# Performance work log

Measured on AMD Instinct MI355X. Metric: run time of the kernel, lower is better.

Reference implementation:

```python
import jax, jax.numpy as jnp
import numpy as np

NUM_HEADS = 8


def setup_inputs() -> dict:
    key = jax.random.key(0)
    k1, k2, k3, k4 = jax.random.split(key, 4)
    C = 256
    x = jax.random.normal(k1, (1, C, 16, 16, 16), dtype=jnp.float32)
    qkv_w = jax.random.normal(k2, (3 * C, C), dtype=jnp.float32) * (C ** -0.5)
    proj_w = jax.random.normal(k3, (C, C), dtype=jnp.float32) * (C ** -0.5)
    proj_b = jax.random.normal(k4, (C,), dtype=jnp.float32) * 0.02
    return {"x": x, "qkv_w": qkv_w, "proj_w": proj_w, "proj_b": proj_b}


def reference(x, qkv_w, proj_w, proj_b):
    B, C, H, W, D = x.shape
    N = H * W * D
    nh = NUM_HEADS
    hd = C // nh
    scale = hd ** -0.5

    xf = x.reshape(B, C, N)
    # 1x1x1 Conv3d == pointwise linear over channel dim
    qkv = jnp.einsum('oc,bcn->bon', qkv_w, xf)           # [B, 3C, N]
    qkv = qkv.reshape(B, 3, nh, hd, N)
    q, k, v = qkv[:, 0], qkv[:, 1], qkv[:, 2]            # each [B, nh, hd, N]

    # q @ k^T over head_dim: scores [B, nh, N, N]
    attn = jnp.einsum('bhdn,bhdm->bhnm', q, k) * scale
    attn = jax.nn.softmax(attn, axis=-1)

    # (attn @ v) then transpose(2,3): result laid out as [B, nh, hd, N]
    out = jnp.einsum('bhnm,bhdm->bhdn', attn, v)
    out = out.reshape(B, C, N)

    out = jnp.einsum('oc,bcn->bon', proj_w, out) + proj_b[None, :, None]
    return out.reshape(B, C, H, W, D)
```

## Files before the change

### kernel.cpp

```cpp
#include <hip/hip_runtime.h>
#include <hip/hip_bf16.h>

typedef short short8 __attribute__((ext_vector_type(8)));
typedef unsigned short ushort8 __attribute__((ext_vector_type(8)));
typedef float f32x4 __attribute__((ext_vector_type(4)));
typedef unsigned int u32x4 __attribute__((ext_vector_type(4)));

#define MFMA16(a, b, c) __builtin_amdgcn_mfma_f32_16x16x32_bf16(a, b, c, 0, 0, 0)

__device__ __forceinline__ unsigned short f2bf(float f) {
    unsigned int u = __float_as_uint(f);
    unsigned int r = (u + 0x7fffu + ((u >> 16) & 1u)) >> 16;
    return (unsigned short)r;
}

__device__ __forceinline__ float fexp2(float x) {
#if __has_builtin(__builtin_amdgcn_exp2f)
    return __builtin_amdgcn_exp2f(x);
#else
    return exp2f(x);
#endif
}

__device__ __forceinline__ unsigned int cvtpk(float lo, float hi) {
    unsigned int r;
    asm("v_cvt_pk_bf16_f32 %0, %1, %2" : "=v"(r) : "v"(lo), "v"(hi));
    return r;
}

__device__ __forceinline__ float hsum4(f32x4 a) { return (a[0] + a[1]) + (a[2] + a[3]); }

#define QSC (0.17677669529663687f * 1.4426950408889634f)

__global__ __launch_bounds__(256) void k_prep(const float* __restrict__ qkv_w,
                                              const float* __restrict__ proj_w,
                                              const float* __restrict__ x,
                                              unsigned short* __restrict__ wqb,
                                              unsigned short* __restrict__ pwb,
                                              unsigned short* __restrict__ xtb) {
    __shared__ float lds[64][65];
    int t = threadIdx.x;
    if (blockIdx.x < 256) {
        int i = (blockIdx.x * 256 + t) * 4;
        const int NQ = 768 * 256;
        const float* src;
        unsigned short* dst;
        if (i < NQ) { src = qkv_w + i; dst = wqb + i; }
        else        { src = proj_w + (i - NQ); dst = pwb + (i - NQ); }
        float4 v = *reinterpret_cast<const float4*>(src);
        ushort4 p;
        p.x = f2bf(v.x); p.y = f2bf(v.y); p.z = f2bf(v.z); p.w = f2bf(v.w);
        *reinterpret_cast<ushort4*>(dst) = p;
        return;
    }
    int bid = blockIdx.x - 256;
    int nt = bid & 63;
    int ct = bid >> 6;
    {
        int cc = t >> 2, nseg = t & 3;
        const float* src = x + (ct * 64 + cc) * 4096 + nt * 64 + nseg * 16;
#pragma unroll
        for (int k2 = 0; k2 < 4; ++k2) {
            float4 v = *reinterpret_cast<const float4*>(src + 4 * k2);
            lds[cc][nseg * 16 + 4 * k2 + 0] = v.x;
            lds[cc][nseg * 16 + 4 * k2 + 1] = v.y;
            lds[cc][nseg * 16 + 4 * k2 + 2] = v.z;
            lds[cc][nseg * 16 + 4 * k2 + 3] = v.w;
        }
    }
    __syncthreads();
    {
        int nn = t >> 2, seg = t & 3;
        unsigned short o[16];
#pragma unroll
        for (int j = 0; j < 16; ++j) o[j] = f2bf(lds[seg * 16 + j][nn]);
        unsigned short* dst = xtb + (nt * 64 + nn) * 256 + ct * 64 + seg * 16;
#pragma unroll
        for (int k2 = 0; k2 < 4; ++k2) {
            ushort4 p;
            p.x = o[4 * k2 + 0]; p.y = o[4 * k2 + 1]; p.z = o[4 * k2 + 2]; p.w = o[4 * k2 + 3];
            *reinterpret_cast<ushort4*>(dst + 4 * k2) = p;
        }
    }
}

__global__ __launch_bounds__(256) void k_qkv(const unsigned short* __restrict__ wqb,
                                             const unsigned short* __restrict__ xtb,
                                             unsigned short* __restrict__ qws,
                                             unsigned short* __restrict__ kws,
                                             unsigned short* __restrict__ vws) {
    int nt = blockIdx.x;
    int ot = blockIdx.y;
    int w = threadIdx.x >> 6;
    int l = threadIdx.x & 63;
    int lr = l & 15, lg = l >> 4;
    int obase = ot * 128 + w * 32;
    int nbase = nt * 64;

    f32x4 acc[2][4];
#pragma unroll
    for (int mi = 0; mi < 2; ++mi)
#pragma unroll
        for (int ni = 0; ni < 4; ++ni) acc[mi][ni] = (f32x4){0.f, 0.f, 0.f, 0.f};

#pragma unroll
    for (int ks = 0; ks < 8; ++ks) {
        short8 a[2], b[4];
#pragma unroll
        for (int mi = 0; mi < 2; ++mi)
            a[mi] = *reinterpret_cast<const short8*>(wqb + (obase + mi * 16 + lr) * 256 + ks * 32 + lg * 8);
#pragma unroll
        for (int ni = 0; ni < 4; ++ni)
            b[ni] = *reinterpret_cast<const short8*>(xtb + (nbase + ni * 16 + lr) * 256 + ks * 32 + lg * 8);
#pragma unroll
        for (int mi = 0; mi < 2; ++mi)
#pragma unroll
            for (int ni = 0; ni < 4; ++ni)
                acc[mi][ni] = MFMA16(a[mi], b[ni], acc[mi][ni]);
    }

#pragma unroll
    for (int mi = 0; mi < 2; ++mi) {
        int o0 = obase + mi * 16 + lg * 4;
#pragma unroll
        for (int ni = 0; ni < 4; ++ni) {
            int n = nbase + ni * 16 + lr;
            f32x4 v = acc[mi][ni];
            if (o0 < 512) {
                float sc = (o0 < 256) ? QSC : 1.0f;
                unsigned short* base = (o0 < 256) ? qws : kws;
                int oo = o0 & 255;
                int h = oo >> 5, d0 = oo & 31;
                ushort4 pk;
                pk.x = f2bf(v[0] * sc); pk.y = f2bf(v[1] * sc);
                pk.z = f2bf(v[2] * sc); pk.w = f2bf(v[3] * sc);
                *reinterpret_cast<ushort4*>(base + h * 131072 + n * 32 + d0) = pk;
            } else {
                int oo = o0 - 512;
#pragma unroll
                for (int r = 0; r < 4; ++r) vws[(oo + r) * 4096 + n] = f2bf(v[r]);
            }
        }
    }
}

__global__ __launch_bounds__(256, 4) void k_attn(const unsigned short* __restrict__ qws,
                                                 const unsigned short* __restrict__ kws,
                                                 const unsigned short* __restrict__ vws,
                                                 float* __restrict__ opart,
                                                 float* __restrict__ oml) {
    __shared__ __align__(16) unsigned short sbuf[4096];

    int h  = blockIdx.x;
    int qs = blockIdx.y;
    int sp = blockIdx.z;
    int t = threadIdx.x;
    int w = t >> 6, l = t & 63, lr = l & 15, lg = l >> 4;

    const unsigned short* qh = qws + h * 131072;
    const unsigned short* kh = kws + h * 131072;
    const unsigned short* vh = vws + h * 131072;

    int qb = qs * 128 + w * 32;
    short8 bq0 = *reinterpret_cast<const short8*>(qh + (qb + lr) * 32 + lg * 8);
    short8 bq1 = *reinterpret_cast<const short8*>(qh + (qb + 16 + lr) * 32 + lg * 8);

    f32x4 o00 = {0.f,0.f,0.f,0.f}, o01 = o00, o10 = o00, o11 = o00;
    f32x4 la0 = {0.f,0.f,0.f,0.f}, la1 = {0.f,0.f,0.f,0.f};

    int krow_s = 8 * (lr >> 2) + (lr & 3) + 4 * (w & 1) + 32 * (w >> 1);
    const unsigned short* ksrc = kh + krow_s * 32 + lg * 8;
    unsigned short* kslot = &sbuf[w * 512 + l * 8];
    const unsigned short* vsrc = vh + ((w & 1) * 16 + lr) * 4096 + (w >> 1) * 32 + lg * 8;
    unsigned short* vslot = &sbuf[2048 + w * 512 + l * 8];

    int mt0 = sp * 16, mt1 = mt0 + 16;

    ushort8 kreg = *reinterpret_cast<const ushort8*>(ksrc + mt0 * 2048);
    ushort8 vreg = *reinterpret_cast<const ushort8*>(vsrc + mt0 * 64);

    for (int mt = mt0; mt < mt1; ++mt) {
        __syncthreads();
        *reinterpret_cast<ushort8*>(kslot) = kreg;
        *reinterpret_cast<ushort8*>(vslot) = vreg;
        __syncthreads();

        if (mt + 1 < mt1) {
            kreg = *reinterpret_cast<const ushort8*>(ksrc + (mt + 1) * 2048);
            vreg = *reinterpret_cast<const ushort8*>(vsrc + (mt + 1) * 64);
        }

        const unsigned short* kb = sbuf;
        short8 ka0 = *reinterpret_cast<const short8*>(kb + l * 8);
        short8 ka1 = *reinterpret_cast<const short8*>(kb + 512 + l * 8);
        short8 ka2 = *reinterpret_cast<const short8*>(kb + 1024 + l * 8);
        short8 ka3 = *reinterpret_cast<const short8*>(kb + 1536 + l * 8);
        const unsigned short* vbp = kb + 2048;
        short8 va00 = *reinterpret_cast<const short8*>(vbp + l * 8);
        short8 va10 = *reinterpret_cast<const short8*>(vbp + 512 + l * 8);
        short8 va01 = *reinterpret_cast<const short8*>(vbp + 1024 + l * 8);
        short8 va11 = *reinterpret_cast<const short8*>(vbp + 1536 + l * 8);

        const f32x4 z = {0.f, 0.f, 0.f, 0.f};
        f32x4 s00 = MFMA16(ka0, bq0, z);
        f32x4 s01 = MFMA16(ka1, bq0, z);
        f32x4 s02 = MFMA16(ka2, bq0, z);
        f32x4 s03 = MFMA16(ka3, bq0, z);
        f32x4 s10 = MFMA16(ka0, bq1, z);
        f32x4 s11 = MFMA16(ka1, bq1, z);
        f32x4 s12 = MFMA16(ka2, bq1, z);
        f32x4 s13 = MFMA16(ka3, bq1, z);

#pragma unroll
        for (int e = 0; e < 4; ++e) {
            s00[e] = fexp2(s00[e]); s01[e] = fexp2(s01[e]);
            s02[e] = fexp2(s02[e]); s03[e] = fexp2(s03[e]);
        }
        la0 += (s00 + s01) + (s02 + s03);
        union { u32x4 u; short8 s8; } p00, p01, p10, p11;
        p00.u[0] = cvtpk(s00[0], s00[1]); p00.u[1] = cvtpk(s00[2], s00[3]);
        p00.u[2] = cvtpk(s01[0], s01[1]); p00.u[3] = cvtpk(s01[2], s01[3]);
        p01.u[0] = cvtpk(s02[0], s02[1]); p01.u[1] = cvtpk(s02[2], s02[3]);
        p01.u[2] = cvtpk(s03[0], s03[1]); p01.u[3] = cvtpk(s03[2], s03[3]);

#pragma unroll
        for (int e = 0; e < 4; ++e) {
            s10[e] = fexp2(s10[e]); s11[e] = fexp2(s11[e]);
            s12[e] = fexp2(s12[e]); s13[e] = fexp2(s13[e]);
        }
        la1 += (s10 + s11) + (s12 + s13);
        p10.u[0] = cvtpk(s10[0], s10[1]); p10.u[1] = cvtpk(s10[2], s10[3]);
        p10.u[2] = cvtpk(s11[0], s11[1]); p10.u[3] = cvtpk(s11[2], s11[3]);
        p11.u[0] = cvtpk(s12[0], s12[1]); p11.u[1] = cvtpk(s12[2], s12[3]);
        p11.u[2] = cvtpk(s13[0], s13[1]); p11.u[3] = cvtpk(s13[2], s13[3]);

        o00 = MFMA16(va00, p00.s8, o00);
        o00 = MFMA16(va01, p01.s8, o00);
        o01 = MFMA16(va10, p00.s8, o01);
        o01 = MFMA16(va11, p01.s8, o01);
        o10 = MFMA16(va00, p10.s8, o10);
        o10 = MFMA16(va01, p11.s8, o10);
        o11 = MFMA16(va10, p10.s8, o11);
        o11 = MFMA16(va11, p11.s8, o11);
    }

    float ls0 = hsum4(la0);
    ls0 += __shfl_xor(ls0, 16);
    ls0 += __shfl_xor(ls0, 32);
    float ls1 = hsum4(la1);
    ls1 += __shfl_xor(ls1, 16);
    ls1 += __shfl_xor(ls1, 32);

    int q0 = qb + lr, q1 = qb + 16 + lr;
    float* ob0 = opart + ((h * 4096 + q0) * 4 + sp) * 32;
    float* ob1 = opart + ((h * 4096 + q1) * 4 + sp) * 32;
    __builtin_nontemporal_store(o00, reinterpret_cast<f32x4*>(ob0 + lg * 4));
    __builtin_nontemporal_store(o01, reinterpret_cast<f32x4*>(ob0 + 16 + lg * 4));
    __builtin_nontemporal_store(o10, reinterpret_cast<f32x4*>(ob1 + lg * 4));
    __builtin_nontemporal_store(o11, reinterpret_cast<f32x4*>(ob1 + 16 + lg * 4));
    oml[(h * 4096 + q0) * 4 + sp] = ls0;
    oml[(h * 4096 + q1) * 4 + sp] = ls1;
}

__global__ __launch_bounds__(256) void k_comb(const float* __restrict__ opart,
                                              const float* __restrict__ oml,
                                              unsigned short* __restrict__ ao) {
    int t = blockIdx.x * 256 + threadIdx.x;
    int hq = t >> 2;
    int dg = (t & 3) * 8;
    f32x4 lv = *reinterpret_cast<const f32x4*>(oml + hq * 4);
    float inv = 1.0f / ((lv[0] + lv[1]) + (lv[2] + lv[3]));

    const float* ob = opart + hq * 128 + dg;
    f32x4 v0 = __builtin_nontemporal_load(reinterpret_cast<const f32x4*>(ob));
    f32x4 v1 = __builtin_nontemporal_load(reinterpret_cast<const f32x4*>(ob + 32));
    f32x4 v2 = __builtin_nontemporal_load(reinterpret_cast<const f32x4*>(ob + 64));
    f32x4 v3 = __builtin_nontemporal_load(reinterpret_cast<const f32x4*>(ob + 96));
    f32x4 acc0 = (v0 + v1) + (v2 + v3);
    v0 = __builtin_nontemporal_load(reinterpret_cast<const f32x4*>(ob + 4));
    v1 = __builtin_nontemporal_load(reinterpret_cast<const f32x4*>(ob + 36));
    v2 = __builtin_nontemporal_load(reinterpret_cast<const f32x4*>(ob + 68));
    v3 = __builtin_nontemporal_load(reinterpret_cast<const f32x4*>(ob + 100));
    f32x4 acc1 = (v0 + v1) + (v2 + v3);

    int h = hq >> 12, q = hq & 4095;
    unsigned short* dst = ao + q * 256 + h * 32 + dg;
    ushort4 pk;
    pk.x = f2bf(acc0[0] * inv); pk.y = f2bf(acc0[1] * inv);
    pk.z = f2bf(acc0[2] * inv); pk.w = f2bf(acc0[3] * inv);
    *reinterpret_cast<ushort4*>(dst) = pk;
    pk.x = f2bf(acc1[0] * inv); pk.y = f2bf(acc1[1] * inv);
    pk.z = f2bf(acc1[2] * inv); pk.w = f2bf(acc1[3] * inv);
    *reinterpret_cast<ushort4*>(dst + 4) = pk;
}

__global__ __launch_bounds__(256) void k_proj(const unsigned short* __restrict__ pwb,
                                              const unsigned short* __restrict__ ao,
                                              const float* __restrict__ bias,
                                              float* __restrict__ out) {
    int nt = blockIdx.x;
    int ot = blockIdx.y;
    int w = threadIdx.x >> 6;
    int l = threadIdx.x & 63;
    int lr = l & 15, lg = l >> 4;
    int obase = ot * 128 + w * 32;
    int nbase = nt * 64;

    f32x4 acc[2][4];
#pragma unroll
    for (int mi = 0; mi < 2; ++mi)
#pragma unroll
        for (int ni = 0; ni < 4; ++ni) acc[mi][ni] = (f32x4){0.f, 0.f, 0.f, 0.f};

#pragma unroll
    for (int ks = 0; ks < 8; ++ks) {
        short8 a[2], b[4];
#pragma unroll
        for (int mi = 0; mi < 2; ++mi)
            a[mi] = *reinterpret_cast<const short8*>(pwb + (obase + mi * 16 + lr) * 256 + ks * 32 + lg * 8);
#pragma unroll
        for (int ni = 0; ni < 4; ++ni)
            b[ni] = *reinterpret_cast<const short8*>(ao + (nbase + ni * 16 + lr) * 256 + ks * 32 + lg * 8);
#pragma unroll
        for (int mi = 0; mi < 2; ++mi)
#pragma unroll
            for (int ni = 0; ni < 4; ++ni)
                acc[mi][ni] = MFMA16(a[mi], b[ni], acc[mi][ni]);
    }

#pragma unroll
    for (int mi = 0; mi < 2; ++mi) {
        int o0 = obase + mi * 16 + lg * 4;
        float b0 = bias[o0 + 0], b1 = bias[o0 + 1], b2 = bias[o0 + 2], b3 = bias[o0 + 3];
#pragma unroll
        for (int ni = 0; ni < 4; ++ni) {
            int n = nbase + ni * 16 + lr;
            out[(o0 + 0) * 4096 + n] = acc[mi][ni][0] + b0;
            out[(o0 + 1) * 4096 + n] = acc[mi][ni][1] + b1;
            out[(o0 + 2) * 4096 + n] = acc[mi][ni][2] + b2;
            out[(o0 + 3) * 4096 + n] = acc[mi][ni][3] + b3;
        }
    }
}

extern "C" void kernel_launch(void* const* d_in, const int* in_sizes, int n_in,
                              void* d_out, int out_size, void* d_ws, size_t ws_size,
                              hipStream_t stream) {
    const float* x      = (const float*)d_in[0];
    const float* qkv_w  = (const float*)d_in[1];
    const float* proj_w = (const float*)d_in[2];
    const float* proj_b = (const float*)d_in[3];
    float* out = (float*)d_out;

    char* ws = (char*)d_ws;
    unsigned short* wqb = (unsigned short*)(ws + 0);
    unsigned short* pwb = (unsigned short*)(ws + 393216);
    unsigned short* xtb = (unsigned short*)(ws + 524288);
    unsigned short* qws = (unsigned short*)(ws + 2621440);
    unsigned short* kws = (unsigned short*)(ws + 4718592);
    unsigned short* vws = (unsigned short*)(ws + 6815744);
    unsigned short* ao  = (unsigned short*)(ws + 8912896);
    float* opart        = (float*)(ws + 11010048);
    float* oml          = (float*)(ws + 27787264);

    k_prep<<<512, 256, 0, stream>>>(qkv_w, proj_w, x, wqb, pwb, xtb);
    k_qkv<<<dim3(64, 6), 256, 0, stream>>>(wqb, xtb, qws, kws, vws);
    k_attn<<<dim3(8, 32, 4), 256, 0, stream>>>(qws, kws, vws, opart, oml);
    k_comb<<<512, 256, 0, stream>>>(opart, oml, ao);
    k_proj<<<dim3(64, 2), 256, 0, stream>>>(pwb, ao, proj_b, out);
}
```

Before: 62.48 us.

## Drop split-KV in attention and fuse combine step into attention epilogue

The attention kernel no longer splits the key dimension four ways. Each block now walks all 64 key tiles and normalizes its own output, writing bf16 results straight to the projection input. This removes the fp32 partial-output buffer, its round trip through global memory and the separate combine launch. The cost is a grid four times smaller (256 blocks) with longer serial loops per block, which lowers parallelism across the many compute units. The occupancy hint of 4 blocks per SM is also removed from the launch bounds.

Result: slower. 70.76 us (+13.2%).

```diff
diff --git a/kernel.cpp b/kernel.cpp
--- a/kernel.cpp
+++ b/kernel.cpp
@@ -144,16 +144,14 @@
     }
 }
 
-__global__ __launch_bounds__(256, 4) void k_attn(const unsigned short* __restrict__ qws,
-                                                 const unsigned short* __restrict__ kws,
-                                                 const unsigned short* __restrict__ vws,
-                                                 float* __restrict__ opart,
-                                                 float* __restrict__ oml) {
+__global__ __launch_bounds__(256) void k_attn(const unsigned short* __restrict__ qws,
+                                              const unsigned short* __restrict__ kws,
+                                              const unsigned short* __restrict__ vws,
+                                              unsigned short* __restrict__ ao) {
     __shared__ __align__(16) unsigned short sbuf[4096];
 
     int h  = blockIdx.x;
     int qs = blockIdx.y;
-    int sp = blockIdx.z;
     int t = threadIdx.x;
     int w = t >> 6, l = t & 63, lr = l & 15, lg = l >> 4;
 
@@ -170,22 +168,20 @@
 
     int krow_s = 8 * (lr >> 2) + (lr & 3) + 4 * (w & 1) + 32 * (w >> 1);
     const unsigned short* ksrc = kh + krow_s * 32 + lg * 8;
+    const unsigned short* vsrc = vh + ((w & 1) * 16 + lr) * 4096 + (w >> 1) * 32 + lg * 8;
     unsigned short* kslot = &sbuf[w * 512 + l * 8];
-    const unsigned short* vsrc = vh + ((w & 1) * 16 + lr) * 4096 + (w >> 1) * 32 + lg * 8;
     unsigned short* vslot = &sbuf[2048 + w * 512 + l * 8];
 
-    int mt0 = sp * 16, mt1 = mt0 + 16;
-
-    ushort8 kreg = *reinterpret_cast<const ushort8*>(ksrc + mt0 * 2048);
-    ushort8 vreg = *reinterpret_cast<const ushort8*>(vsrc + mt0 * 64);
-
-    for (int mt = mt0; mt < mt1; ++mt) {
+    ushort8 kreg = *reinterpret_cast<const ushort8*>(ksrc);
+    ushort8 vreg = *reinterpret_cast<const ushort8*>(vsrc);
+
+    for (int mt = 0; mt < 64; ++mt) {
         __syncthreads();
         *reinterpret_cast<ushort8*>(kslot) = kreg;
         *reinterpret_cast<ushort8*>(vslot) = vreg;
         __syncthreads();
 
-        if (mt + 1 < mt1) {
+        if (mt + 1 < 64) {
             kreg = *reinterpret_cast<const ushort8*>(ksrc + (mt + 1) * 2048);
             vreg = *reinterpret_cast<const ushort8*>(vsrc + (mt + 1) * 64);
         }
@@ -250,48 +246,23 @@
     float ls1 = hsum4(la1);
     ls1 += __shfl_xor(ls1, 16);
     ls1 += __shfl_xor(ls1, 32);
+    float inv0 = 1.0f / ls0;
+    float inv1 = 1.0f / ls1;
 
     int q0 = qb + lr, q1 = qb + 16 + lr;
-    float* ob0 = opart + ((h * 4096 + q0) * 4 + sp) * 32;
-    float* ob1 = opart + ((h * 4096 + q1) * 4 + sp) * 32;
-    __builtin_nontemporal_store(o00, reinterpret_cast<f32x4*>(ob0 + lg * 4));
-    __builtin_nontemporal_store(o01, reinterpret_cast<f32x4*>(ob0 + 16 + lg * 4));
-    __builtin_nontemporal_store(o10, reinterpret_cast<f32x4*>(ob1 + lg * 4));
-    __builtin_nontemporal_store(o11, reinterpret_cast<f32x4*>(ob1 + 16 + lg * 4));
-    oml[(h * 4096 + q0) * 4 + sp] = ls0;
-    oml[(h * 4096 + q1) * 4 + sp] = ls1;
-}
-
-__global__ __launch_bounds__(256) void k_comb(const float* __restrict__ opart,
-                                              const float* __restrict__ oml,
-                                              unsigned short* __restrict__ ao) {
-    int t = blockIdx.x * 256 + threadIdx.x;
-    int hq = t >> 2;
-    int dg = (t & 3) * 8;
-    f32x4 lv = *reinterpret_cast<const f32x4*>(oml + hq * 4);
-    float inv = 1.0f / ((lv[0] + lv[1]) + (lv[2] + lv[3]));
-
-    const float* ob = opart + hq * 128 + dg;
-    f32x4 v0 = __builtin_nontemporal_load(reinterpret_cast<const f32x4*>(ob));
-    f32x4 v1 = __builtin_nontemporal_load(reinterpret_cast<const f32x4*>(ob + 32));
-    f32x4 v2 = __builtin_nontemporal_load(reinterpret_cast<const f32x4*>(ob + 64));
-    f32x4 v3 = __builtin_nontemporal_load(reinterpret_cast<const f32x4*>(ob + 96));
-    f32x4 acc0 = (v0 + v1) + (v2 + v3);
-    v0 = __builtin_nontemporal_load(reinterpret_cast<const f32x4*>(ob + 4));
-    v1 = __builtin_nontemporal_load(reinterpret_cast<const f32x4*>(ob + 36));
-    v2 = __builtin_nontemporal_load(reinterpret_cast<const f32x4*>(ob + 68));
-    v3 = __builtin_nontemporal_load(reinterpret_cast<const f32x4*>(ob + 100));
-    f32x4 acc1 = (v0 + v1) + (v2 + v3);
-
-    int h = hq >> 12, q = hq & 4095;
-    unsigned short* dst = ao + q * 256 + h * 32 + dg;
-    ushort4 pk;
-    pk.x = f2bf(acc0[0] * inv); pk.y = f2bf(acc0[1] * inv);
-    pk.z = f2bf(acc0[2] * inv); pk.w = f2bf(acc0[3] * inv);
-    *reinterpret_cast<ushort4*>(dst) = pk;
-    pk.x = f2bf(acc1[0] * inv); pk.y = f2bf(acc1[1] * inv);
-    pk.z = f2bf(acc1[2] * inv); pk.w = f2bf(acc1[3] * inv);
-    *reinterpret_cast<ushort4*>(dst + 4) = pk;
+    int c0 = h * 32 + lg * 4;
+    unsigned int pk0 = cvtpk(o00[0] * inv0, o00[1] * inv0);
+    unsigned int pk1 = cvtpk(o00[2] * inv0, o00[3] * inv0);
+    *reinterpret_cast<uint2*>(ao + q0 * 256 + c0) = make_uint2(pk0, pk1);
+    pk0 = cvtpk(o01[0] * inv0, o01[1] * inv0);
+    pk1 = cvtpk(o01[2] * inv0, o01[3] * inv0);
+    *reinterpret_cast<uint2*>(ao + q0 * 256 + c0 + 16) = make_uint2(pk0, pk1);
+    pk0 = cvtpk(o10[0] * inv1, o10[1] * inv1);
+    pk1 = cvtpk(o10[2] * inv1, o10[3] * inv1);
+    *reinterpret_cast<uint2*>(ao + q1 * 256 + c0) = make_uint2(pk0, pk1);
+    pk0 = cvtpk(o11[0] * inv1, o11[1] * inv1);
+    pk1 = cvtpk(o11[2] * inv1, o11[3] * inv1);
+    *reinterpret_cast<uint2*>(ao + q1 * 256 + c0 + 16) = make_uint2(pk0, pk1);
 }
 
 __global__ __launch_bounds__(256) void k_proj(const unsigned short* __restrict__ pwb,
@@ -360,12 +331,9 @@
     unsigned short* kws = (unsigned short*)(ws + 4718592);
     unsigned short* vws = (unsigned short*)(ws + 6815744);
     unsigned short* ao  = (unsigned short*)(ws + 8912896);
-    float* opart        = (float*)(ws + 11010048);
-    float* oml          = (float*)(ws + 27787264);
 
     k_prep<<<512, 256, 0, stream>>>(qkv_w, proj_w, x, wqb, pwb, xtb);
     k_qkv<<<dim3(64, 6), 256, 0, stream>>>(wqb, xtb, qws, kws, vws);
-    k_attn<<<dim3(8, 32, 4), 256, 0, stream>>>(qws, kws, vws, opart, oml);
-    k_comb<<<512, 256, 0, stream>>>(opart, oml, ao);
+    k_attn<<<dim3(8, 32), 256, 0, stream>>>(qws, kws, vws, ao);
     k_proj<<<dim3(64, 2), 256, 0, stream>>>(pwb, ao, proj_b, out);
 }
```
